# Optimization experiments

Hardware: AMD Instinct MI355X
Metric: run time of the kernel (lower is better)

## Reference

```python
import jax, jax.numpy as jnp
import numpy as np

N = 100000       # patches per slide (bag size)
D = 512          # size[1] for size_arg='big'
D_ATTN = 256     # size[2]
C = 4            # n_classes
N_REFS = 3
TP_RATE = 0.01
NP_RATE = 0.01
REF_RATE = 0.01
EPS = 1e-10


def setup_inputs() -> dict:
    key = jax.random.key(0)
    ks = jax.random.split(key, 8)
    w = lambda k, shape: jax.random.normal(k, shape, jnp.float32) * 0.02
    return {
        "h": jax.random.normal(ks[0], (N, D), jnp.float32),
        "label": jax.random.randint(ks[1], (2,), 0, C),
        "Wa": w(ks[2], (D, D_ATTN)), "ba": jnp.zeros((D_ATTN,), jnp.float32),
        "Wb": w(ks[3], (D, D_ATTN)), "bb": jnp.zeros((D_ATTN,), jnp.float32),
        "Wc": w(ks[4], (D_ATTN, C)), "bc": jnp.zeros((C,), jnp.float32),
        "Wcls": w(ks[5], (D, C)), "bcls": jnp.zeros((C,), jnp.float32),
        "Wr": w(ks[6], (N_REFS, D, C + 1)),
        "br": jnp.zeros((N_REFS, C + 1), jnp.float32),
    }


def _ce(logits, targets):
    # cross entropy with integer targets, reduction='none'
    logp = jax.nn.log_softmax(logits, axis=-1)
    return -jnp.take_along_axis(logp, targets[..., None], axis=-1)[..., 0]


def _find_candidate_loss(final_score, h, in_label, Wr, br):
    n = final_score.shape[0]
    k = max(1, int(n * TP_RATE))
    mn = final_score.min(axis=0)
    mx = final_score.max(axis=0)
    norm = (final_score - mn) / (mx - mn)                     # [N, C]
    vals, idx = jax.lax.top_k(norm.T, k)                      # [C, k]
    valid = (vals > 0.5) & in_label[:, None]                  # only classes in label
    logits = jnp.einsum('ckd,de->cke', h[idx], Wr) + br       # [C, k, C+1]
    tgt = jnp.broadcast_to(jnp.arange(C)[:, None], (C, k))
    ce_tp = _ce(logits, tgt)
    mean_score = final_score.mean(axis=1)
    k_np = int(n * NP_RATE)
    nvals, nidx = jax.lax.top_k(-mean_score, k_np)
    np_valid = (-nvals) < 0.5
    np_logits = h[nidx] @ Wr + br                             # [k_np, C+1]
    ce_np = -jax.nn.log_softmax(np_logits, axis=-1)[:, C]
    num = jnp.sum(ce_tp * valid) + jnp.sum(ce_np * np_valid)
    den = valid.sum() + np_valid.sum()
    return num / jnp.maximum(den, 1)


def _find_candidate_ref_loss(ref_score, h, in_label, Wr, br):
    n = ref_score.shape[0]
    k = max(1, int(n * REF_RATE))
    vals, idx = jax.lax.top_k(ref_score.T, k)                 # [C+1, k]
    include = jnp.concatenate([in_label, jnp.array([True])])  # bg class always included
    valid = (vals > 0.5) & include[:, None]
    logits = jnp.einsum('ckd,de->cke', h[idx], Wr) + br       # [C+1, k, C+1]
    tgt = jnp.broadcast_to(jnp.arange(C + 1)[:, None], (C + 1, k))
    ce = _ce(logits, tgt)
    return jnp.sum(ce * valid) / jnp.maximum(valid.sum(), 1)


def _forward(h, label, Wa, ba, Wb, bb, Wc, bc, Wcls, bcls, Wr, br):
    # gated attention (Attn_Net_Gated), eval mode (dropout off)
    a = jnp.tanh(h @ Wa + ba)
    b = jax.nn.sigmoid(h @ Wb + bb)
    det_logit = (a * b) @ Wc + bc                             # [N, C]
    cls_score = jax.nn.softmax(h @ Wcls + bcls, axis=1)
    det_score = jax.nn.softmax(det_logit, axis=0)             # softmax over instances
    final_score = cls_score * det_score
    in_label = jnp.any(jnp.arange(C)[:, None] == label[None, :], axis=1)  # [C] bool
    instance_loss = jnp.float32(0.0)
    ref_score = final_score
    for r in range(N_REFS):
        if r == 0:
            instance_loss = instance_loss + _find_candidate_loss(final_score, h, in_label, Wr[r], br[r])
        else:
            instance_loss = instance_loss + _find_candidate_ref_loss(ref_score, h, in_label, Wr[r], br[r])
        ref_score = jax.nn.softmax(h @ Wr[r] + br[r], axis=1)  # [N, C+1]
    Y_prob = jnp.clip(jnp.sum(final_score, axis=0), EPS, 1.0 - EPS)
    return final_score, Y_prob, ref_score, instance_loss


def reference(h, label, Wa, ba, Wb, bb, Wc, bc, Wcls, bcls, Wr, br):
    final_score, Y_prob, ref_score, instance_loss = _forward(
        h, label, Wa, ba, Wb, bb, Wc, bc, Wcls, bcls, Wr, br)
    Y_hat = jnp.argmax(Y_prob)[None]
    return final_score, Y_prob, Y_hat, ref_score, instance_loss
```

## Files before the change

### kernel.cpp

```cpp
#include <hip/hip_runtime.h>
#include <math.h>

#define NI    100000
#define KSEL  1000
#define NCOL2 640
#define HBINS 2048

#define OUT_FS   0
#define OUT_YP   400000
#define OUT_YH   400004
#define OUT_REF  400005
#define OUT_LOSS 900005

#define OFF_DET    0
#define OFF_CLS    400000
#define OFF_REF0   800000
#define OFF_REF1   1300000
#define OFF_MEAN   1800000
#define OFF_WPT    1900000
#define OFF_BPACK  2063840
#define OFF_SCAL   2064480
#define OFF_SELIDX 2064608
#define OFF_HIST   2079608

#define SC_SUMEXP 0
#define SC_YPROB  4
#define SC_FSMIN  8
#define SC_FSMAX  12
#define SC_THR    16
#define SC_INCL   20
#define SC_NUM    25
#define SC_CNT    28
#define SC_PREFIX 43
#define SC_RESTK  58

typedef short short8 __attribute__((ext_vector_type(8)));
typedef float f32x4 __attribute__((ext_vector_type(4)));

__device__ __forceinline__ unsigned fenc(float x) {
    unsigned u = __float_as_uint(x);
    return (u & 0x80000000u) ? ~u : (u | 0x80000000u);
}
__device__ __forceinline__ unsigned short f2bf(float f) {
    unsigned u = __float_as_uint(f);
    return (unsigned short)((u + 0x7FFFu + ((u >> 16) & 1u)) >> 16);
}

__global__ __launch_bounds__(256) void prep_kernel(
    const float* __restrict__ Wa, const float* __restrict__ Wb,
    const float* __restrict__ Wcls, const float* __restrict__ Wr,
    const float* __restrict__ ba, const float* __restrict__ bb,
    const float* __restrict__ bcls, const float* __restrict__ br,
    float* __restrict__ ws)
{
    const int tid0 = blockIdx.x * 256 + threadIdx.x;
    unsigned short* wpT = (unsigned short*)(ws + OFF_WPT);
    if (tid0 < NCOL2 * 512) {
        const int c = tid0 >> 9, k = tid0 & 511;
        float v = 0.f;
        if (c < 512)      { const int j = c >> 1; v = (c & 1) ? Wb[k*256 + j] : Wa[k*256 + j]; }
        else if (c < 516)   v = Wcls[k*4 + (c - 512)];
        else if (c < 531) { const int q = c - 516; v = Wr[((q/5)*512 + k)*5 + (q%5)]; }
        wpT[tid0] = f2bf(v);
    }
    if (tid0 < NCOL2) {
        float v = 0.f; const int c = tid0;
        if (c < 512)      v = (c & 1) ? bb[c >> 1] : ba[c >> 1];
        else if (c < 516) v = bcls[c - 512];
        else if (c < 531) v = br[c - 516];
        ws[OFF_BPACK + c] = v;
    }
    if (tid0 < 128) {
        unsigned* su = (unsigned*)(ws + OFF_SCAL);
        unsigned v = 0u;
        if (tid0 >= SC_FSMIN && tid0 < SC_FSMIN + 4)   v = 0xFFFFFFFFu;
        if (tid0 >= SC_RESTK && tid0 < SC_RESTK + 15)  v = (unsigned)KSEL;
        su[tid0] = v;
    }
    unsigned* hist = (unsigned*)(ws + OFF_HIST);
    if (tid0 < 15 * HBINS) hist[tid0] = 0u;
}

__global__ __launch_bounds__(512, 4) void gemm_mfma(
    const float* __restrict__ h, const unsigned short* __restrict__ wpT,
    const float* __restrict__ bpack, const float* __restrict__ Wc,
    const float* __restrict__ bc,
    float* __restrict__ det_logit, float* __restrict__ det_sumexp,
    float* __restrict__ cls_score, float* __restrict__ ref0,
    float* __restrict__ ref1, float* __restrict__ out_ref2)
{
    __shared__ alignas(16) unsigned char smem[73216];
    float* slog  = (float*)smem;
    float* sbias = (float*)(smem + 65536);
    float* sWc   = (float*)(smem + 68096);
    float* sdet  = (float*)(smem + 72192);

    const int tid  = threadIdx.x;
    const int lane = tid & 63;
    const int w    = tid >> 6;
    const int wm   = (w >> 2) * 32;
    const int wn   = (w & 3) * 32;
    const int lrow = lane & 15, lq = lane >> 4;
    const int row_base = blockIdx.x * 64;

    for (int t = tid; t < 640;  t += 512) sbias[t] = bpack[t];
    for (int t = tid; t < 1024; t += 512) sWc[t]   = Wc[t];
    if (tid < 64) { sdet[tid*4+0] = 0.f; sdet[tid*4+1] = 0.f; sdet[tid*4+2] = 0.f; sdet[tid*4+3] = 0.f; }

    #pragma unroll
    for (int pass = 0; pass < 2; ++pass) {
        float4 tmp[8];
        #pragma unroll
        for (int it = 0; it < 8; ++it) {
            const int q = (pass*8 + it)*512 + tid;
            const int r = q >> 7, c4 = q & 127;
            const int grow = row_base + r;
            tmp[it] = (grow < NI) ? *(const float4*)&h[(size_t)grow * 512 + c4*4]
                                  : make_float4(0.f, 0.f, 0.f, 0.f);
        }
        #pragma unroll
        for (int it = 0; it < 8; ++it) {
            const int q = (pass*8 + it)*512 + tid;
            const int r = q >> 7, c4 = q & 127;
            const int s = (c4 >> 1) ^ (r & 7);
            ushort4 pk;
            pk.x = f2bf(tmp[it].x); pk.y = f2bf(tmp[it].y);
            pk.z = f2bf(tmp[it].z); pk.w = f2bf(tmp[it].w);
            *(ushort4*)(smem + r*1024 + (s<<4) + ((c4&1)<<3)) = pk;
        }
    }
    __syncthreads();

    const int row0 = wm + lrow;
    const int r7   = row0 & 7;
    const unsigned abase = (unsigned)(row0*1024 + ((lq ^ (r7 & 3)) << 4));
    const unsigned x64   = (unsigned)((r7 & 4) << 4);

    for (int cb = 0; cb < 5; ++cb) {
        const int n0 = cb * 128;
        const unsigned short* bp0 = wpT + (size_t)(n0 + wn + lrow) * 512 + lq*8;
        const unsigned short* bp1 = bp0 + 16*512;

        f32x4 acc[2][2];
        #pragma unroll
        for (int mt = 0; mt < 2; ++mt)
            #pragma unroll
            for (int nt = 0; nt < 2; ++nt) acc[mt][nt] = (f32x4)0.f;

        uint4 bb0[3], bb1[3];
        bb0[0] = *(const uint4*)(bp0);      bb1[0] = *(const uint4*)(bp1);
        bb0[1] = *(const uint4*)(bp0+32);   bb1[1] = *(const uint4*)(bp1+32);
        bb0[2] = *(const uint4*)(bp0+64);   bb1[2] = *(const uint4*)(bp1+64);

        #pragma unroll
        for (int s = 0; s < 16; ++s) {
            const int kc = s * 32;
            const uint4 b0 = bb0[s % 3];
            const uint4 b1 = bb1[s % 3];
            if (s + 3 < 16) {
                bb0[s % 3] = *(const uint4*)(bp0 + kc + 96);
                bb1[s % 3] = *(const uint4*)(bp1 + kc + 96);
            }
            const unsigned aoff = abase + (((unsigned)(kc*2)) ^ x64);
            const short8 af0 = *(const short8*)(smem + aoff);
            const short8 af1 = *(const short8*)(smem + aoff + 16384);
            acc[0][0] = __builtin_amdgcn_mfma_f32_16x16x32_bf16(af0, *(const short8*)&b0, acc[0][0], 0, 0, 0);
            acc[0][1] = __builtin_amdgcn_mfma_f32_16x16x32_bf16(af0, *(const short8*)&b1, acc[0][1], 0, 0, 0);
            acc[1][0] = __builtin_amdgcn_mfma_f32_16x16x32_bf16(af1, *(const short8*)&b0, acc[1][0], 0, 0, 0);
            acc[1][1] = __builtin_amdgcn_mfma_f32_16x16x32_bf16(af1, *(const short8*)&b1, acc[1][1], 0, 0, 0);
        }

        if (cb < 4) {
            #pragma unroll
            for (int mt = 0; mt < 2; ++mt) {
                #pragma unroll
                for (int reg = 0; reg < 4; ++reg) {
                    float c0 = 0.f, c1 = 0.f, c2 = 0.f, c3 = 0.f;
                    #pragma unroll
                    for (int nt = 0; nt < 2; ++nt) {
                        const int cl = wn + nt*16 + lrow;
                        const float v = acc[mt][nt][reg] + sbias[n0 + cl];
                        const float p = __shfl_xor(v, 1);
                        const float ve = (lane & 1) ? p : v;
                        const float vo = (lane & 1) ? v : p;
                        const float e2 = __expf(2.f * ve);
                        const float gate = (1.f - 2.f / (e2 + 1.f)) * (1.f / (1.f + __expf(-vo)));
                        if (!(lane & 1)) {
                            const int j = (n0 + cl) >> 1;
                            c0 += gate * sWc[j*4+0]; c1 += gate * sWc[j*4+1];
                            c2 += gate * sWc[j*4+2]; c3 += gate * sWc[j*4+3];
                        }
                    }
                    #pragma unroll
                    for (int m = 1; m <= 8; m <<= 1) {
                        c0 += __shfl_xor(c0, m); c1 += __shfl_xor(c1, m);
                        c2 += __shfl_xor(c2, m); c3 += __shfl_xor(c3, m);
                    }
                    if ((lane & 15) == 0) {
                        const int rl = wm + mt*16 + lq*4 + reg;
                        atomicAdd(&sdet[rl*4+0], c0); atomicAdd(&sdet[rl*4+1], c1);
                        atomicAdd(&sdet[rl*4+2], c2); atomicAdd(&sdet[rl*4+3], c3);
                    }
                }
            }
        } else {
            __syncthreads();
            if ((w & 3) == 0) {
                #pragma unroll
                for (int mt = 0; mt < 2; ++mt)
                    #pragma unroll
                    for (int reg = 0; reg < 4; ++reg)
                        #pragma unroll
                        for (int nt = 0; nt < 2; ++nt) {
                            const int cl = nt*16 + lrow;
                            if (cl < 19) {
                                const int row = wm + mt*16 + lq*4 + reg;
                                slog[row * 20 + cl] = acc[mt][nt][reg] + sbias[512 + cl];
                            }
                        }
            }
            __syncthreads();
            if (tid < 64) {
                const int grow = row_base + tid;
                if (grow < NI) {
                    float L[19];
                    #pragma unroll
                    for (int q = 0; q < 19; ++q) L[q] = slog[tid * 20 + q];
                    {
                        float m = fmaxf(fmaxf(L[0], L[1]), fmaxf(L[2], L[3]));
                        float e0 = __expf(L[0]-m), e1 = __expf(L[1]-m), e2 = __expf(L[2]-m), e3 = __expf(L[3]-m);
                        const float inv = 1.f / (e0 + e1 + e2 + e3);
                        cls_score[(size_t)grow*4+0] = e0*inv; cls_score[(size_t)grow*4+1] = e1*inv;
                        cls_score[(size_t)grow*4+2] = e2*inv; cls_score[(size_t)grow*4+3] = e3*inv;
                    }
                    #pragma unroll
                    for (int r = 0; r < 3; ++r) {
                        float m = L[4+5*r];
                        #pragma unroll
                        for (int e = 1; e < 5; ++e) m = fmaxf(m, L[4+5*r+e]);
                        float ev[5]; float s = 0.f;
                        #pragma unroll
                        for (int e = 0; e < 5; ++e) { ev[e] = __expf(L[4+5*r+e] - m); s += ev[e]; }
                        const float inv = 1.f / s;
                        float* dst = (r == 0) ? ref0 : ((r == 1) ? ref1 : out_ref2);
                        #pragma unroll
                        for (int e = 0; e < 5; ++e) dst[(size_t)grow*5+e] = ev[e] * inv;
                    }
                }
            }
        }
    }
    __syncthreads();

    if (w == 0) {
        const int grow = row_base + tid;
        float e0 = 0.f, e1 = 0.f, e2 = 0.f, e3 = 0.f;
        const float d0 = sdet[tid*4+0] + bc[0];
        const float d1 = sdet[tid*4+1] + bc[1];
        const float d2 = sdet[tid*4+2] + bc[2];
        const float d3 = sdet[tid*4+3] + bc[3];
        if (grow < NI) {
            float4 dv = make_float4(d0, d1, d2, d3);
            *(float4*)&det_logit[(size_t)grow * 4] = dv;
            e0 = __expf(d0); e1 = __expf(d1); e2 = __expf(d2); e3 = __expf(d3);
        }
        #pragma unroll
        for (int m = 1; m < 64; m <<= 1) {
            e0 += __shfl_xor(e0, m); e1 += __shfl_xor(e1, m);
            e2 += __shfl_xor(e2, m); e3 += __shfl_xor(e3, m);
        }
        if (lane == 0) {
            atomicAdd(&det_sumexp[0], e0); atomicAdd(&det_sumexp[1], e1);
            atomicAdd(&det_sumexp[2], e2); atomicAdd(&det_sumexp[3], e3);
        }
    }
}

__global__ __launch_bounds__(256) void final_kernel(const float* __restrict__ det_logit,
        const float* __restrict__ cls_score, const float* __restrict__ det_sumexp,
        float* __restrict__ out_fs, float* __restrict__ mean_sc, float* __restrict__ yprob_sum,
        unsigned* __restrict__ fs_min_enc, unsigned* __restrict__ fs_max_enc)
{
    __shared__ float ssum[4][4], smin[4][4], smax[4][4];
    const int i = blockIdx.x * 256 + threadIdx.x;
    const bool valid = i < NI;
    float f[4]; float tot = 0.f;
    #pragma unroll
    for (int c = 0; c < 4; ++c) {
        float v = 0.f;
        if (valid) {
            const float ds = __expf(det_logit[(size_t)i*4+c]) / det_sumexp[c];
            v = cls_score[(size_t)i*4+c] * ds;
            out_fs[(size_t)i*4+c] = v;
        }
        f[c] = v; tot += v;
    }
    if (valid) mean_sc[i] = 0.25f * tot;
    float sm[4], mn[4], mx[4];
    #pragma unroll
    for (int c = 0; c < 4; ++c) {
        sm[c] = f[c];
        mn[c] = valid ? f[c] : 3.4e38f;
        mx[c] = valid ? f[c] : -3.4e38f;
    }
    #pragma unroll
    for (int c = 0; c < 4; ++c)
        #pragma unroll
        for (int m = 1; m < 64; m <<= 1) {
            sm[c] += __shfl_xor(sm[c], m, 64);
            mn[c] = fminf(mn[c], __shfl_xor(mn[c], m, 64));
            mx[c] = fmaxf(mx[c], __shfl_xor(mx[c], m, 64));
        }
    const int w = threadIdx.x >> 6;
    if ((threadIdx.x & 63) == 0) {
        #pragma unroll
        for (int c = 0; c < 4; ++c) { ssum[w][c] = sm[c]; smin[w][c] = mn[c]; smax[w][c] = mx[c]; }
    }
    __syncthreads();
    if (threadIdx.x < 4) {
        const int c = threadIdx.x;
        float S = 0.f, MN = 3.4e38f, MX = -3.4e38f;
        #pragma unroll
        for (int w2 = 0; w2 < 4; ++w2) {
            S += ssum[w2][c]; MN = fminf(MN, smin[w2][c]); MX = fmaxf(MX, smax[w2][c]);
        }
        atomicAdd(&yprob_sum[c], S);
        atomicMin(&fs_min_enc[c], fenc(MN));
        atomicMax(&fs_max_enc[c], fenc(MX));
    }
}

__global__ void scalars_kernel(const int* __restrict__ label, float* __restrict__ out,
                               float* __restrict__ ws_scal)
{
    if (blockIdx.x == 0 && threadIdx.x == 0) {
        float* sf = ws_scal; unsigned* su = (unsigned*)ws_scal; int* si = (int*)ws_scal;
        float best = -1.f; int arg = 0;
        for (int c = 0; c < 4; ++c) {
            float v = sf[SC_YPROB + c];
            v = fminf(fmaxf(v, 1e-10f), 1.f - 1e-10f);
            out[OUT_YP + c] = v;
            if (v > best) { best = v; arg = c; }
        }
        out[OUT_YH] = (float)arg;
        for (int c = 0; c < 4; ++c) {
            unsigned ue = su[SC_FSMIN + c], ux = su[SC_FSMAX + c];
            float mn = (ue & 0x80000000u) ? __uint_as_float(ue & 0x7FFFFFFFu) : __uint_as_float(~ue);
            float mx = (ux & 0x80000000u) ? __uint_as_float(ux & 0x7FFFFFFFu) : __uint_as_float(~ux);
            sf[SC_THR + c] = mn + 0.5f * (mx - mn);
        }
        const int l0 = label[0], l1 = label[1];
        for (int c = 0; c < 4; ++c) si[SC_INCL + c] = (l0 == c || l1 == c) ? 1 : 0;
        si[SC_INCL + 4] = 1;
    }
}

__device__ __forceinline__ float sel_value(int b, int i, const float* fs, const float* mean,
                                           const float* r0, const float* r1) {
    if (b < 4)  return fs[(size_t)i*4 + b];
    if (b == 4) return mean[i];
    if (b < 10) return r0[(size_t)i*5 + (b-5)];
    return r1[(size_t)i*5 + (b-10)];
}

__global__ __launch_bounds__(256) void hist_kernel(const float* __restrict__ fs,
        const float* __restrict__ mean, const float* __restrict__ r0, const float* __restrict__ r1,
        unsigned* __restrict__ hist, const float* __restrict__ ws_scal, int shift, int width)
{
    const int b = blockIdx.x;
    const unsigned* su = (const unsigned*)ws_scal;
    const int* si = (const int*)ws_scal;
    const int c = (b < 4) ? b : ((b == 4) ? -1 : ((b < 10) ? b - 5 : b - 10));
    if (c >= 0 && !si[SC_INCL + c]) return;
    __shared__ unsigned lh[HBINS];
    const int nbins = 1 << width;
    for (int t = threadIdx.x; t < nbins; t += 256) lh[t] = 0u;
    __syncthreads();
    const int pb = shift + width;
    const unsigned prefix = su[SC_PREFIX + b];
    const unsigned mask = (unsigned)(nbins - 1);
    for (int i = blockIdx.y * 256 + threadIdx.x; i < NI; i += 8 * 256) {
        const float v = sel_value(b, i, fs, mean, r0, r1);
        const unsigned u = fenc(b == 4 ? -v : v);
        if (pb >= 32 || (u >> pb) == prefix)
            atomicAdd(&lh[(u >> shift) & mask], 1u);
    }
    __syncthreads();
    for (int t = threadIdx.x; t < nbins; t += 256)
        if (lh[t]) atomicAdd(&hist[(size_t)b * HBINS + t], lh[t]);
}

__global__ __launch_bounds__(256) void scan_kernel(unsigned* __restrict__ hist,
                                                   float* __restrict__ ws_scal, int width)
{
    __shared__ unsigned csum[256];
    const int b = blockIdx.x;
    unsigned* su = (unsigned*)ws_scal;
    unsigned* hh = hist + (size_t)b * HBINS;
    const int nbins = 1 << width;
    const int chunk = (nbins + 255) >> 8;
    unsigned s = 0;
    for (int j = 0; j < chunk; ++j) {
        const int idx = threadIdx.x * chunk + j;
        if (idx < nbins) s += hh[idx];
    }
    csum[threadIdx.x] = s;
    __syncthreads();
    if (threadIdx.x == 0) {
        const unsigned K = su[SC_RESTK + b];
        unsigned running = 0; unsigned found = 0; unsigned rem = K;
        int t;
        for (t = 255; t >= 0; --t) {
            if (running + csum[t] >= K) break;
            running += csum[t];
        }
        if (t < 0) t = 0;
        for (int j = chunk - 1; j >= 0; --j) {
            const int idx = t * chunk + j;
            if (idx >= nbins) continue;
            const unsigned cc = hh[idx];
            if (running + cc >= K) { found = (unsigned)idx; rem = K - running; break; }
            running += cc;
        }
        su[SC_RESTK + b] = rem;
        su[SC_PREFIX + b] = (su[SC_PREFIX + b] << width) | found;
    }
    __syncthreads();
    for (int t2 = threadIdx.x; t2 < nbins; t2 += 256) hh[t2] = 0u;
}

__global__ __launch_bounds__(256) void collect_kernel(const float* __restrict__ fs,
        const float* __restrict__ mean, const float* __restrict__ r0, const float* __restrict__ r1,
        float* __restrict__ ws_scal, int* __restrict__ sel_idx)
{
    const int b = blockIdx.x;
    unsigned* su = (unsigned*)ws_scal; int* si = (int*)ws_scal; float* sf = ws_scal;
    const int c = (b < 4) ? b : ((b == 4) ? -1 : ((b < 10) ? b - 5 : b - 10));
    if (c >= 0 && !si[SC_INCL + c]) return;
    const unsigned kth = su[SC_PREFIX + b];
    const float extra = (b < 4) ? sf[SC_THR + b] : 0.5f;
    for (int i = blockIdx.y * 256 + threadIdx.x; i < NI; i += 8 * 256) {
        const float v = sel_value(b, i, fs, mean, r0, r1);
        const unsigned u = fenc(b == 4 ? -v : v);
        const bool cond = (b == 4) ? (v < 0.5f) : (v > extra);
        if (u >= kth && cond) {
            const int pos = atomicAdd(&si[SC_CNT + b], 1);
            if (pos < KSEL) sel_idx[b * KSEL + pos] = i;
        }
    }
}

__global__ __launch_bounds__(256) void ce_kernel(const float* __restrict__ h,
        const float* __restrict__ Wr, const float* __restrict__ br,
        const int* __restrict__ sel_idx, float* __restrict__ ws_scal)
{
    const int* si = (const int*)ws_scal;
    float* sf = ws_scal;
    const int lane = threadIdx.x & 63;
    const int wid = (blockIdx.x * blockDim.x + threadIdx.x) >> 6;
    const int nw = (gridDim.x * blockDim.x) >> 6;
    float l0a = 0.f, l1a = 0.f, l2a = 0.f;
    for (int slot = wid; slot < 15 * KSEL; slot += nw) {
        const int b = slot / KSEL;
        const int j = slot - b * KSEL;
        const int cnt = min(si[SC_CNT + b], KSEL);
        if (j >= cnt) continue;
        const int i = sel_idx[b * KSEL + j];
        const int g = (b < 5) ? 0 : ((b < 10) ? 1 : 2);
        const int tgt = (b < 4) ? b : ((b == 4) ? 4 : ((b < 10) ? (b - 5) : (b - 10)));
        const float* hr = h + (size_t)i * 512;
        const float* wr = Wr + (size_t)g * 512 * 5;
        const int d0 = lane * 8;
        const float4 va = *(const float4*)&hr[d0];
        const float4 vb = *(const float4*)&hr[d0 + 4];
        const float hv[8] = {va.x, va.y, va.z, va.w, vb.x, vb.y, vb.z, vb.w};
        float acc[5] = {0.f, 0.f, 0.f, 0.f, 0.f};
        #pragma unroll
        for (int t = 0; t < 8; ++t) {
            const float* row = wr + (size_t)(d0 + t) * 5;
            #pragma unroll
            for (int e = 0; e < 5; ++e) acc[e] += hv[t] * row[e];
        }
        #pragma unroll
        for (int e = 0; e < 5; ++e)
            #pragma unroll
            for (int m = 1; m < 64; m <<= 1) acc[e] += __shfl_xor(acc[e], m, 64);
        if (lane == 0) {
            float l[5];
            #pragma unroll
            for (int e = 0; e < 5; ++e) l[e] = acc[e] + br[g * 5 + e];
            float mx = l[0];
            #pragma unroll
            for (int e = 1; e < 5; ++e) mx = fmaxf(mx, l[e]);
            float s = 0.f;
            #pragma unroll
            for (int e = 0; e < 5; ++e) s += __expf(l[e] - mx);
            const float ce = logf(s) + mx - l[tgt];
            if (g == 0) l0a += ce; else if (g == 1) l1a += ce; else l2a += ce;
        }
    }
    if (lane == 0) {
        if (l0a != 0.f) atomicAdd(&sf[SC_NUM + 0], l0a);
        if (l1a != 0.f) atomicAdd(&sf[SC_NUM + 1], l1a);
        if (l2a != 0.f) atomicAdd(&sf[SC_NUM + 2], l2a);
    }
}

__global__ void loss_kernel(const float* __restrict__ ws_scal, float* __restrict__ out)
{
    if (blockIdx.x == 0 && threadIdx.x == 0) {
        const int* si = (const int*)ws_scal;
        float loss = 0.f;
        for (int g = 0; g < 3; ++g) {
            int den = 0;
            for (int b = g * 5; b < g * 5 + 5; ++b) den += min(si[SC_CNT + b], KSEL);
            loss += ws_scal[SC_NUM + g] / (float)(den > 1 ? den : 1);
        }
        out[OUT_LOSS] = loss;
    }
}

extern "C" void kernel_launch(void* const* d_in, const int* in_sizes, int n_in,
                              void* d_out, int out_size, void* d_ws, size_t ws_size,
                              hipStream_t stream)
{
    const float* h    = (const float*)d_in[0];
    const int*   lab  = (const int*)d_in[1];
    const float* Wa   = (const float*)d_in[2];
    const float* ba   = (const float*)d_in[3];
    const float* Wb   = (const float*)d_in[4];
    const float* bb   = (const float*)d_in[5];
    const float* Wc   = (const float*)d_in[6];
    const float* bc   = (const float*)d_in[7];
    const float* Wcls = (const float*)d_in[8];
    const float* bcls = (const float*)d_in[9];
    const float* Wr   = (const float*)d_in[10];
    const float* br   = (const float*)d_in[11];
    float* out = (float*)d_out;
    float* ws  = (float*)d_ws;

    float* det_logit = ws + OFF_DET;
    float* cls_score = ws + OFF_CLS;
    float* ref0      = ws + OFF_REF0;
    float* ref1      = ws + OFF_REF1;
    float* mean_sc   = ws + OFF_MEAN;
    unsigned short* wpT = (unsigned short*)(ws + OFF_WPT);
    float* scal = ws + OFF_SCAL;
    int*   sel_idx = (int*)(ws + OFF_SELIDX);
    unsigned* hist = (unsigned*)(ws + OFF_HIST);

    hipLaunchKernelGGL(prep_kernel, dim3(1280), dim3(256), 0, stream,
                       Wa, Wb, Wcls, Wr, ba, bb, bcls, br, ws);
    hipLaunchKernelGGL(gemm_mfma, dim3(1563), dim3(512), 0, stream,
                       h, wpT, ws + OFF_BPACK, Wc, bc,
                       det_logit, scal + SC_SUMEXP, cls_score, ref0, ref1, out + OUT_REF);
    hipLaunchKernelGGL(final_kernel, dim3(391), dim3(256), 0, stream,
                       det_logit, cls_score, scal + SC_SUMEXP,
                       out + OUT_FS, mean_sc, scal + SC_YPROB,
                       (unsigned*)(scal) + SC_FSMIN, (unsigned*)(scal) + SC_FSMAX);
    hipLaunchKernelGGL(scalars_kernel, dim3(1), dim3(64), 0, stream, lab, out, scal);
    hipLaunchKernelGGL(hist_kernel, dim3(15, 8), dim3(256), 0, stream,
                       out + OUT_FS, mean_sc, ref0, ref1, hist, scal, 21, 11);
    hipLaunchKernelGGL(scan_kernel, dim3(15), dim3(256), 0, stream, hist, scal, 11);
    hipLaunchKernelGGL(hist_kernel, dim3(15, 8), dim3(256), 0, stream,
                       out + OUT_FS, mean_sc, ref0, ref1, hist, scal, 10, 11);
    hipLaunchKernelGGL(scan_kernel, dim3(15), dim3(256), 0, stream, hist, scal, 11);
    hipLaunchKernelGGL(hist_kernel, dim3(15, 8), dim3(256), 0, stream,
                       out + OUT_FS, mean_sc, ref0, ref1, hist, scal, 0, 10);
    hipLaunchKernelGGL(scan_kernel, dim3(15), dim3(256), 0, stream, hist, scal, 10);
    hipLaunchKernelGGL(collect_kernel, dim3(15, 8), dim3(256), 0, stream,
                       out + OUT_FS, mean_sc, ref0, ref1, scal, sel_idx);
    hipLaunchKernelGGL(ce_kernel, dim3(240), dim3(256), 0, stream, h, Wr, br, sel_idx, scal);
    hipLaunchKernelGGL(loss_kernel, dim3(1), dim3(64), 0, stream, scal, out);
}
```

Before: 737.6 us.

## Compute gated-attention det projection with MFMA instead of shuffles and LDS atomics

The gated tanh*sigmoid values are written as bf16 into a swizzled LDS tile. The projection onto Wc is then done with an extra bf16 MFMA per column block, using a Wc transpose packed into the unused weight columns 600-607. This replaces the per-row shuffle reductions and shared-memory float atomics. The B-fragment prefetch depth grows from 3 to 4, and the A fragments are now double-buffered from LDS. The cost is two extra block barriers per column block, bf16 rounding of the gate values, and more LDS.

```diff
diff --git a/kernel.cpp b/kernel.cpp
--- a/kernel.cpp
+++ b/kernel.cpp
@@ -49,6 +49,7 @@
 __global__ __launch_bounds__(256) void prep_kernel(
     const float* __restrict__ Wa, const float* __restrict__ Wb,
     const float* __restrict__ Wcls, const float* __restrict__ Wr,
+    const float* __restrict__ Wc,
     const float* __restrict__ ba, const float* __restrict__ bb,
     const float* __restrict__ bcls, const float* __restrict__ br,
     float* __restrict__ ws)
@@ -61,6 +62,11 @@
         if (c < 512)      { const int j = c >> 1; v = (c & 1) ? Wb[k*256 + j] : Wa[k*256 + j]; }
         else if (c < 516)   v = Wcls[k*4 + (c - 512)];
         else if (c < 531) { const int q = c - 516; v = Wr[((q/5)*512 + k)*5 + (q%5)]; }
+        else if (c >= 600 && c < 608) {
+            const int q2 = (c - 600)*512 + k;
+            const int cc = q2 >> 8, j = q2 & 255;
+            v = (cc < 4) ? Wc[j*4 + cc] : 0.f;
+        }
         wpT[tid0] = f2bf(v);
     }
     if (tid0 < NCOL2) {
@@ -83,17 +89,15 @@
 
 __global__ __launch_bounds__(512, 4) void gemm_mfma(
     const float* __restrict__ h, const unsigned short* __restrict__ wpT,
-    const float* __restrict__ bpack, const float* __restrict__ Wc,
-    const float* __restrict__ bc,
+    const float* __restrict__ bpack, const float* __restrict__ bc,
     float* __restrict__ det_logit, float* __restrict__ det_sumexp,
     float* __restrict__ cls_score, float* __restrict__ ref0,
     float* __restrict__ ref1, float* __restrict__ out_ref2)
 {
-    __shared__ alignas(16) unsigned char smem[73216];
-    float* slog  = (float*)smem;
-    float* sbias = (float*)(smem + 65536);
-    float* sWc   = (float*)(smem + 68096);
-    float* sdet  = (float*)(smem + 72192);
+    __shared__ alignas(16) unsigned char smem[77312];
+    float* slog  = (float*)(smem + 65536);
+    float* detxf = (float*)(smem + 73728);
+    float* sbias = (float*)(smem + 74752);
 
     const int tid  = threadIdx.x;
     const int lane = tid & 63;
@@ -102,10 +106,9 @@
     const int wn   = (w & 3) * 32;
     const int lrow = lane & 15, lq = lane >> 4;
     const int row_base = blockIdx.x * 64;
+    const unsigned short* wct = wpT + 600*512;
 
     for (int t = tid; t < 640;  t += 512) sbias[t] = bpack[t];
-    for (int t = tid; t < 1024; t += 512) sWc[t]   = Wc[t];
-    if (tid < 64) { sdet[tid*4+0] = 0.f; sdet[tid*4+1] = 0.f; sdet[tid*4+2] = 0.f; sdet[tid*4+3] = 0.f; }
 
     #pragma unroll
     for (int pass = 0; pass < 2; ++pass) {
@@ -136,6 +139,10 @@
     const unsigned abase = (unsigned)(row0*1024 + ((lq ^ (r7 & 3)) << 4));
     const unsigned x64   = (unsigned)((r7 & 4) << 4);
 
+    const int rt = w >> 1, ks = w & 1;
+    const unsigned gaoff = 65536u + (unsigned)((rt*16 + lrow)*128 + (((ks*4 + lq) ^ (lrow & 7)) << 4));
+    f32x4 acc_det = (f32x4)0.f;
+
     for (int cb = 0; cb < 5; ++cb) {
         const int n0 = cb * 128;
         const unsigned short* bp0 = wpT + (size_t)(n0 + wn + lrow) * 512 + lq*8;
@@ -147,37 +154,42 @@
             #pragma unroll
             for (int nt = 0; nt < 2; ++nt) acc[mt][nt] = (f32x4)0.f;
 
-        uint4 bb0[3], bb1[3];
-        bb0[0] = *(const uint4*)(bp0);      bb1[0] = *(const uint4*)(bp1);
-        bb0[1] = *(const uint4*)(bp0+32);   bb1[1] = *(const uint4*)(bp1+32);
-        bb0[2] = *(const uint4*)(bp0+64);   bb1[2] = *(const uint4*)(bp1+64);
+        uint4 bb0[4], bb1[4];
+        #pragma unroll
+        for (int i = 0; i < 4; ++i) {
+            bb0[i] = *(const uint4*)(bp0 + i*32);
+            bb1[i] = *(const uint4*)(bp1 + i*32);
+        }
+        short8 afn0 = *(const short8*)(smem + (abase ^ x64));
+        short8 afn1 = *(const short8*)(smem + (abase ^ x64) + 16384);
 
         #pragma unroll
         for (int s = 0; s < 16; ++s) {
-            const int kc = s * 32;
-            const uint4 b0 = bb0[s % 3];
-            const uint4 b1 = bb1[s % 3];
-            if (s + 3 < 16) {
-                bb0[s % 3] = *(const uint4*)(bp0 + kc + 96);
-                bb1[s % 3] = *(const uint4*)(bp1 + kc + 96);
+            const uint4 b0 = bb0[s & 3];
+            const uint4 b1 = bb1[s & 3];
+            if (s + 4 < 16) {
+                bb0[s & 3] = *(const uint4*)(bp0 + (s + 4)*32);
+                bb1[s & 3] = *(const uint4*)(bp1 + (s + 4)*32);
             }
-            const unsigned aoff = abase + (((unsigned)(kc*2)) ^ x64);
-            const short8 af0 = *(const short8*)(smem + aoff);
-            const short8 af1 = *(const short8*)(smem + aoff + 16384);
-            acc[0][0] = __builtin_amdgcn_mfma_f32_16x16x32_bf16(af0, *(const short8*)&b0, acc[0][0], 0, 0, 0);
-            acc[0][1] = __builtin_amdgcn_mfma_f32_16x16x32_bf16(af0, *(const short8*)&b1, acc[0][1], 0, 0, 0);
-            acc[1][0] = __builtin_amdgcn_mfma_f32_16x16x32_bf16(af1, *(const short8*)&b0, acc[1][0], 0, 0, 0);
-            acc[1][1] = __builtin_amdgcn_mfma_f32_16x16x32_bf16(af1, *(const short8*)&b1, acc[1][1], 0, 0, 0);
+            const short8 a0 = afn0, a1 = afn1;
+            if (s + 1 < 16) {
+                const unsigned aoff = abase + (((unsigned)((s + 1)*64)) ^ x64);
+                afn0 = *(const short8*)(smem + aoff);
+                afn1 = *(const short8*)(smem + aoff + 16384);
+            }
+            acc[0][0] = __builtin_amdgcn_mfma_f32_16x16x32_bf16(a0, *(const short8*)&b0, acc[0][0], 0, 0, 0);
+            acc[0][1] = __builtin_amdgcn_mfma_f32_16x16x32_bf16(a0, *(const short8*)&b1, acc[0][1], 0, 0, 0);
+            acc[1][0] = __builtin_amdgcn_mfma_f32_16x16x32_bf16(a1, *(const short8*)&b0, acc[1][0], 0, 0, 0);
+            acc[1][1] = __builtin_amdgcn_mfma_f32_16x16x32_bf16(a1, *(const short8*)&b1, acc[1][1], 0, 0, 0);
         }
 
         if (cb < 4) {
             #pragma unroll
-            for (int mt = 0; mt < 2; ++mt) {
+            for (int mt = 0; mt < 2; ++mt)
                 #pragma unroll
-                for (int reg = 0; reg < 4; ++reg) {
-                    float c0 = 0.f, c1 = 0.f, c2 = 0.f, c3 = 0.f;
+                for (int nt = 0; nt < 2; ++nt)
                     #pragma unroll
-                    for (int nt = 0; nt < 2; ++nt) {
+                    for (int reg = 0; reg < 4; ++reg) {
                         const int cl = wn + nt*16 + lrow;
                         const float v = acc[mt][nt][reg] + sbias[n0 + cl];
                         const float p = __shfl_xor(v, 1);
@@ -186,25 +198,20 @@
                         const float e2 = __expf(2.f * ve);
                         const float gate = (1.f - 2.f / (e2 + 1.f)) * (1.f / (1.f + __expf(-vo)));
                         if (!(lane & 1)) {
-                            const int j = (n0 + cl) >> 1;
-                            c0 += gate * sWc[j*4+0]; c1 += gate * sWc[j*4+1];
-                            c2 += gate * sWc[j*4+2]; c3 += gate * sWc[j*4+3];
+                            const int row = wm + mt*16 + lq*4 + reg;
+                            const int jj  = (wn >> 1) + nt*8 + (lrow >> 1);
+                            *(unsigned short*)(smem + 65536 + row*128 +
+                                (((jj >> 3) ^ (row & 7)) << 4) + ((jj & 7) << 1)) = f2bf(gate);
                         }
                     }
-                    #pragma unroll
-                    for (int m = 1; m <= 8; m <<= 1) {
-                        c0 += __shfl_xor(c0, m); c1 += __shfl_xor(c1, m);
-                        c2 += __shfl_xor(c2, m); c3 += __shfl_xor(c3, m);
-                    }
-                    if ((lane & 15) == 0) {
-                        const int rl = wm + mt*16 + lq*4 + reg;
-                        atomicAdd(&sdet[rl*4+0], c0); atomicAdd(&sdet[rl*4+1], c1);
-                        atomicAdd(&sdet[rl*4+2], c2); atomicAdd(&sdet[rl*4+3], c3);
-                    }
-                }
+            __syncthreads();
+            {
+                const short8 ga = *(const short8*)(smem + gaoff);
+                const short8 gb = *(const short8*)&wct[lrow*256 + cb*64 + ks*32 + lq*8];
+                acc_det = __builtin_amdgcn_mfma_f32_16x16x32_bf16(ga, gb, acc_det, 0, 0, 0);
             }
+            __syncthreads();
         } else {
-            __syncthreads();
             if ((w & 3) == 0) {
                 #pragma unroll
                 for (int mt = 0; mt < 2; ++mt)
@@ -250,29 +257,28 @@
             }
         }
     }
-    __syncthreads();
-
-    if (w == 0) {
-        const int grow = row_base + tid;
-        float e0 = 0.f, e1 = 0.f, e2 = 0.f, e3 = 0.f;
-        const float d0 = sdet[tid*4+0] + bc[0];
-        const float d1 = sdet[tid*4+1] + bc[1];
-        const float d2 = sdet[tid*4+2] + bc[2];
-        const float d3 = sdet[tid*4+3] + bc[3];
-        if (grow < NI) {
-            float4 dv = make_float4(d0, d1, d2, d3);
-            *(float4*)&det_logit[(size_t)grow * 4] = dv;
-            e0 = __expf(d0); e1 = __expf(d1); e2 = __expf(d2); e3 = __expf(d3);
-        }
-        #pragma unroll
-        for (int m = 1; m < 64; m <<= 1) {
-            e0 += __shfl_xor(e0, m); e1 += __shfl_xor(e1, m);
-            e2 += __shfl_xor(e2, m); e3 += __shfl_xor(e3, m);
-        }
-        if (lane == 0) {
-            atomicAdd(&det_sumexp[0], e0); atomicAdd(&det_sumexp[1], e1);
-            atomicAdd(&det_sumexp[2], e2); atomicAdd(&det_sumexp[3], e3);
-        }
+
+    if (ks == 1 && lrow < 4) {
+        #pragma unroll
+        for (int reg = 0; reg < 4; ++reg)
+            detxf[rt*64 + (lq*4 + reg)*4 + lrow] = acc_det[reg];
+    }
+    __syncthreads();
+    if (ks == 0 && lrow < 4) {
+        float e[4];
+        #pragma unroll
+        for (int reg = 0; reg < 4; ++reg) {
+            const int row = rt*16 + lq*4 + reg;
+            const int grow = row_base + row;
+            const float d = acc_det[reg] + detxf[rt*64 + (lq*4 + reg)*4 + lrow] + bc[lrow];
+            if (grow < NI) {
+                det_logit[(size_t)grow*4 + lrow] = d;
+                e[reg] = __expf(d);
+            } else e[reg] = 0.f;
+        }
+        float s = e[0] + e[1] + e[2] + e[3];
+        s += __shfl_xor(s, 16); s += __shfl_xor(s, 32);
+        if (lq == 0) atomicAdd(&det_sumexp[lrow], s);
     }
 }
 
@@ -550,9 +556,9 @@
     unsigned* hist = (unsigned*)(ws + OFF_HIST);
 
     hipLaunchKernelGGL(prep_kernel, dim3(1280), dim3(256), 0, stream,
-                       Wa, Wb, Wcls, Wr, ba, bb, bcls, br, ws);
+                       Wa, Wb, Wcls, Wr, Wc, ba, bb, bcls, br, ws);
     hipLaunchKernelGGL(gemm_mfma, dim3(1563), dim3(512), 0, stream,
-                       h, wpT, ws + OFF_BPACK, Wc, bc,
+                       h, wpT, ws + OFF_BPACK, bc,
                        det_logit, scal + SC_SUMEXP, cls_score, ref0, ref1, out + OUT_REF);
     hipLaunchKernelGGL(final_kernel, dim3(391), dim3(256), 0, stream,
                        det_logit, cls_score, scal + SC_SUMEXP,
```

Result: no change. 738.1 us (+0.1%).
